# Kernel tuning notes

Measured on AMD Instinct MI355X. Metric: run time of the kernel, lower is better.

Reference implementation:

```python
import jax, jax.numpy as jnp
import numpy as np

D_MODEL = 1024
D_STATE = 16
D_CONV = 4
EXPAND = 2
D_INNER = EXPAND * D_MODEL          # 2048
DT_RANK = (D_MODEL + 15) // 16      # 64
B_SZ, L = 2, 2048


def setup_inputs() -> dict:
    key = jax.random.key(0)
    ks = jax.random.split(key, 14)
    s = 0.02
    dt_init = jax.random.uniform(ks[10], (D_INNER,), minval=1e-3, maxval=0.1)
    A = jnp.tile(jnp.arange(1, D_STATE + 1, dtype=jnp.float32)[None, :], (D_INNER, 1))
    return {
        "x_f": jax.random.normal(ks[0], (B_SZ, L, D_MODEL), jnp.float32),
        "x_h": jax.random.normal(ks[1], (B_SZ, L, D_MODEL), jnp.float32),
        "W_hf": s * jax.random.normal(ks[2], (D_MODEL, D_MODEL), jnp.float32),
        "b_hf": jnp.zeros((D_MODEL,), jnp.float32),
        "W_in": s * jax.random.normal(ks[3], (2 * D_INNER, D_MODEL), jnp.float32),
        "conv_w": s * jax.random.normal(ks[4], (D_INNER, 1, D_CONV), jnp.float32),
        "conv_b": jnp.zeros((D_INNER,), jnp.float32),
        "W_x": s * jax.random.normal(ks[5], (DT_RANK + 2 * D_STATE, D_INNER), jnp.float32),
        "W_dt": (DT_RANK ** -0.5) * jax.random.normal(ks[6], (D_INNER, DT_RANK), jnp.float32),
        "b_dt": jnp.log(jnp.expm1(dt_init)),
        "A_log": jnp.log(A),
        "D": jnp.ones((D_INNER,), jnp.float32),
        "W_out": s * jax.random.normal(ks[7], (D_MODEL, D_INNER), jnp.float32),
    }


def _mamba(x, W_in, conv_w, conv_b, W_x, W_dt, b_dt, A_log, D, W_out):
    B, Lx, _ = x.shape
    # in_proj -> x, z branches  [B, L, 2*d_inner]
    xz = jnp.einsum("bld,ed->ble", x, W_in)
    x_in, z = jnp.split(xz, 2, axis=-1)
    # causal depthwise conv1d, kernel d_conv, groups = d_inner
    x_nch = jnp.transpose(x_in, (0, 2, 1))  # [B, d_inner, L]
    x_conv = jax.lax.conv_general_dilated(
        x_nch, conv_w, window_strides=(1,), padding=[(D_CONV - 1, 0)],
        dimension_numbers=("NCH", "OIH", "NCH"), feature_group_count=D_INNER)
    x_c = jax.nn.silu(jnp.transpose(x_conv, (0, 2, 1)) + conv_b)  # [B, L, d_inner]
    # input-dependent dt, B, C
    x_dbl = jnp.einsum("ble,fe->blf", x_c, W_x)
    dt_r = x_dbl[..., :DT_RANK]
    B_ssm = x_dbl[..., DT_RANK:DT_RANK + D_STATE]          # [B, L, d_state]
    C_ssm = x_dbl[..., DT_RANK + D_STATE:]                  # [B, L, d_state]
    dt = jax.nn.softplus(jnp.einsum("blr,er->ble", dt_r, W_dt) + b_dt)  # [B, L, d_inner]
    A = -jnp.exp(A_log)  # [d_inner, d_state]

    # selective scan over time; carry h: [B, d_inner, d_state]
    def step(h, inp):
        dt_t, B_t, C_t, x_t = inp  # [B,d_inner], [B,d_state], [B,d_state], [B,d_inner]
        dA = jnp.exp(dt_t[:, :, None] * A)                       # [B, d_inner, d_state]
        dBx = dt_t[:, :, None] * B_t[:, None, :] * x_t[:, :, None]
        h = dA * h + dBx
        y_t = jnp.einsum("bes,bs->be", h, C_t)
        return h, y_t

    seq = (jnp.transpose(dt, (1, 0, 2)), jnp.transpose(B_ssm, (1, 0, 2)),
           jnp.transpose(C_ssm, (1, 0, 2)), jnp.transpose(x_c, (1, 0, 2)))
    h0 = jnp.zeros((B, D_INNER, D_STATE), x.dtype)
    _, ys = jax.lax.scan(step, h0, seq)
    y = jnp.transpose(ys, (1, 0, 2)) + D * x_c   # skip term
    y = y * jax.nn.silu(z)                        # output gate
    return jnp.einsum("ble,de->bld", y, W_out)


def reference(x_f, x_h, W_hf, b_hf, W_in, conv_w, conv_b, W_x, W_dt, b_dt, A_log, D, W_out):
    hf_gate = jax.nn.sigmoid(jnp.einsum("bld,ed->ble", x_h, W_hf) + b_hf)
    modulated = x_f * hf_gate
    return _mamba(modulated, W_in, conv_w, conv_b, W_x, W_dt, b_dt, A_log, D, W_out)
```

## Files before the change

kernel.cpp:

```cpp
#include <hip/hip_runtime.h>
#include <hip/hip_bf16.h>
#include <math.h>

#define L_SEQ  2048
#define BATCH  2
#define DMODEL 1024
#define DINNER 2048
#define DSTATE 16
#define NCHUNK 32
#define LCH    (L_SEQ / NCHUNK)

typedef __attribute__((ext_vector_type(8))) short bf16x8;
typedef __attribute__((ext_vector_type(4))) float f32x4;

__device__ __forceinline__ unsigned short f2bu(float x) {
    __hip_bfloat16 h = __float2bfloat16(x);
    return __builtin_bit_cast(unsigned short, h);
}
__device__ __forceinline__ float fast_exp2(float x) {
    float r; asm("v_exp_f32 %0, %1" : "=v"(r) : "v"(x)); return r;
}
#define LOG2E 1.44269504088896f

__global__ __launch_bounds__(256) void cvt_all(
    const float* __restrict__ Wout, const float* __restrict__ Win,
    const float* __restrict__ xh,   const float* __restrict__ Whf,
    const float* __restrict__ Wx,   const float* __restrict__ Wdt,
    __hip_bfloat16* __restrict__ dWout, __hip_bfloat16* __restrict__ dWin,
    __hip_bfloat16* __restrict__ dxh,   __hip_bfloat16* __restrict__ dWhf,
    __hip_bfloat16* __restrict__ dWx,   __hip_bfloat16* __restrict__ dWdt)
{
    int bid = blockIdx.x;
    const float* s; __hip_bfloat16* d;
    if (bid < 2048)       { s = Wout; d = dWout; }
    else if (bid < 6144)  { s = Win;  d = dWin;  bid -= 2048; }
    else if (bid < 10240) { s = xh;   d = dxh;   bid -= 6144; }
    else if (bid < 11264) { s = Whf;  d = dWhf;  bid -= 10240; }
    else if (bid < 11520) {
        bid -= 11264;
        const int i = (bid * 256 + threadIdx.x) * 4;
        const int r = i >> 11;
        ushort4 u = {0, 0, 0, 0};
        if (r < 96) {
            const float4 v = *reinterpret_cast<const float4*>(&Wx[i]);
            u.x = f2bu(v.x); u.y = f2bu(v.y); u.z = f2bu(v.z); u.w = f2bu(v.w);
        }
        *reinterpret_cast<ushort4*>(&dWx[i]) = u;
        return;
    }
    else                  { s = Wdt;  d = dWdt;  bid -= 11520; }
    const int i = (bid * 256 + threadIdx.x) * 4;
    const float4 v = *reinterpret_cast<const float4*>(&s[i]);
    ushort4 u;
    u.x = f2bu(v.x); u.y = f2bu(v.y); u.z = f2bu(v.z); u.w = f2bu(v.w);
    *reinterpret_cast<ushort4*>(&d[i]) = u;
}

template <int EPI>
__global__ __launch_bounds__(256) void mfma_gemm(
    const __hip_bfloat16* __restrict__ A, int lda,
    const __hip_bfloat16* __restrict__ Bw, int ldb,
    int ksz,
    float* __restrict__ Cf, int ldc,
    __hip_bfloat16* __restrict__ Cb,
    __hip_bfloat16* __restrict__ Cb2,
    const float* __restrict__ bias,
    const float* __restrict__ mul, int ldmul)
{
    __shared__ unsigned short As[64 * 32];
    __shared__ unsigned short Bs[128 * 32];
    const int tid = threadIdx.x;
    const int row0 = blockIdx.y * 64;
    const int col0 = blockIdx.x * 128;
    const int wid = tid >> 6, lane = tid & 63;
    const int wr = wid >> 1, wc = wid & 1;
    const int fr = lane & 15, fq = lane >> 4;
    const int kz0 = blockIdx.z * ksz;

    f32x4 acc[2][4];
#pragma unroll
    for (int i = 0; i < 2; i++)
#pragma unroll
        for (int j = 0; j < 4; j++) acc[i][j] = (f32x4){0.f, 0.f, 0.f, 0.f};

    const size_t ga  = (size_t)(row0 + (tid >> 2)) * lda + (tid & 3) * 8;
    const size_t gb0 = (size_t)(col0 + (tid >> 2)) * ldb + (tid & 3) * 8;
    const size_t gb1 = (size_t)(col0 + 64 + (tid >> 2)) * ldb + (tid & 3) * 8;
    const int nk = ksz >> 5;

    for (int kk = 0; kk < nk; kk++) {
        const int koff = kz0 + kk * 32;
#if __has_builtin(__builtin_amdgcn_global_load_lds)
        __syncthreads();
        __builtin_amdgcn_global_load_lds(
            (const __attribute__((address_space(1))) unsigned int*)(A + ga + koff),
            (__attribute__((address_space(3))) unsigned int*)&As[tid * 8], 16, 0, 0);
        __builtin_amdgcn_global_load_lds(
            (const __attribute__((address_space(1))) unsigned int*)(Bw + gb0 + koff),
            (__attribute__((address_space(3))) unsigned int*)&Bs[tid * 8], 16, 0, 0);
        __builtin_amdgcn_global_load_lds(
            (const __attribute__((address_space(1))) unsigned int*)(Bw + gb1 + koff),
            (__attribute__((address_space(3))) unsigned int*)&Bs[2048 + tid * 8], 16, 0, 0);
        __syncthreads();
#else
        const uint4 va  = *reinterpret_cast<const uint4*>(A + ga + koff);
        const uint4 vb0 = *reinterpret_cast<const uint4*>(Bw + gb0 + koff);
        const uint4 vb1 = *reinterpret_cast<const uint4*>(Bw + gb1 + koff);
        __syncthreads();
        *reinterpret_cast<uint4*>(&As[tid * 8]) = va;
        *reinterpret_cast<uint4*>(&Bs[tid * 8]) = vb0;
        *reinterpret_cast<uint4*>(&Bs[2048 + tid * 8]) = vb1;
        __syncthreads();
#endif
        bf16x8 af[2], bq[4];
#pragma unroll
        for (int rb = 0; rb < 2; rb++)
            af[rb] = *reinterpret_cast<const bf16x8*>(
                &As[(wr * 32 + rb * 16 + fr) * 32 + fq * 8]);
#pragma unroll
        for (int cb = 0; cb < 4; cb++)
            bq[cb] = *reinterpret_cast<const bf16x8*>(
                &Bs[(wc * 64 + cb * 16 + fr) * 32 + fq * 8]);
#pragma unroll
        for (int rb = 0; rb < 2; rb++)
#pragma unroll
            for (int cb = 0; cb < 4; cb++)
                acc[rb][cb] = __builtin_amdgcn_mfma_f32_16x16x32_bf16(
                    af[rb], bq[cb], acc[rb][cb], 0, 0, 0);
    }

    float* Cz = Cf;
    if (EPI == 0)
        Cz = Cf + (size_t)blockIdx.z * (size_t)(gridDim.y * 64) * ldc;
    const int r0 = row0 + wr * 32, c0 = col0 + wc * 64;
#pragma unroll
    for (int rb = 0; rb < 2; rb++)
#pragma unroll
        for (int cb = 0; cb < 4; cb++) {
            const int col = c0 + cb * 16 + fr;
#pragma unroll
            for (int j = 0; j < 4; j++) {
                const int row = r0 + rb * 16 + fq * 4 + j;
                float v = acc[rb][cb][j];
                if (EPI == 0) {
                    Cz[(size_t)row * ldc + col] = v;
                } else if (EPI == 1) {
                    v = 1.f / (1.f + __expf(-(v + bias[col])));
                    v *= mul[(size_t)row * ldmul + col];
                    Cb[(size_t)row * ldc + col] = __float2bfloat16(v);
                } else if (EPI == 2) {
                    if (col0 < 2048) Cb[(size_t)row * 2048 + col] = __float2bfloat16(v);
                    else             Cb2[(size_t)row * 2048 + col - 2048] = __float2bfloat16(v);
                } else {
                    v += bias[col];
                    v = (v > 20.f) ? v : log1pf(__expf(v));
                    Cb[(size_t)row * ldc + col] = __float2bfloat16(v);
                }
            }
        }
}

__global__ __launch_bounds__(256) void reduce_xdbl(
    const float* __restrict__ part, float* __restrict__ xdbl,
    __hip_bfloat16* __restrict__ dtr)
{
    const int i = blockIdx.x * 256 + threadIdx.x;
    float s = 0.f;
#pragma unroll
    for (int j = 0; j < 8; j++) s += part[(size_t)j * 524288 + i];
    xdbl[i] = s;
    const int col = i & 127;
    if (col < 64) dtr[((i >> 7) << 6) + col] = __float2bfloat16(s);
}

__global__ __launch_bounds__(256) void conv_silu_kernel(
    const __hip_bfloat16* __restrict__ xin_b, const float* __restrict__ cw,
    const float* __restrict__ cb, __hip_bfloat16* __restrict__ xcb)
{
    int gid = blockIdx.x * 256 + threadIdx.x;
    int e = gid & (DINNER - 1);
    int row = gid >> 11;
    int t = row & (L_SEQ - 1);
    float s = cb[e];
#pragma unroll
    for (int j = 0; j < 4; j++) {
        int tt = t - 3 + j;
        if (tt >= 0)
            s = fmaf(cw[e * 4 + j],
                     __bfloat162float(xin_b[(size_t)(row - 3 + j) * 2048 + e]), s);
    }
    xcb[(size_t)row * 2048 + e] = __float2bfloat16(s / (1.f + __expf(-s)));
}

__global__ __launch_bounds__(256) void scan_pass_a(
    const __hip_bfloat16* __restrict__ dtb, const __hip_bfloat16* __restrict__ xcb,
    const float* __restrict__ xdbl, const float* __restrict__ A_log,
    float* __restrict__ hloc, float* __restrict__ Pp)
{
    __shared__ float sB[LCH][16];
    const int tid = threadIdx.x;
    const int e = (blockIdx.x << 8) + tid;
    const int chunk = blockIdx.y;
    const int b = blockIdx.z;
    const int t0 = chunk * LCH;

    {
        const int r = tid >> 2, sl = tid & 3;
        *(float4*)&sB[r][sl * 4] =
            *(const float4*)&xdbl[(size_t)(b * L_SEQ + t0 + r) * 128 + 64 + sl * 4];
    }
    float av[16];
#pragma unroll
    for (int sq = 0; sq < 4; sq++) {
        const float4 al = *(const float4*)&A_log[e * 16 + sq * 4];
#pragma unroll
        for (int j = 0; j < 4; j++)
            av[sq * 4 + j] = -fast_exp2(((const float*)&al)[j] * LOG2E);
    }
    float h[16];
#pragma unroll
    for (int s = 0; s < 16; s++) h[s] = 0.f;
    float sdt = 0.f;
    __syncthreads();

    const size_t rb = (size_t)(b * L_SEQ + t0) * 2048 + e;
    float dtv_n = __bfloat162float(dtb[rb]);
    float xv_n = __bfloat162float(xcb[rb]);
    for (int t = 0; t < LCH; t++) {
        const float dtv = dtv_n, xv = xv_n;
        if (t + 1 < LCH) {
            dtv_n = __bfloat162float(dtb[rb + (size_t)(t + 1) * 2048]);
            xv_n = __bfloat162float(xcb[rb + (size_t)(t + 1) * 2048]);
        }
        sdt += dtv;
        const float dtx = dtv * xv;
        const float dl2 = dtv * LOG2E;
#pragma unroll
        for (int sq = 0; sq < 4; sq++) {
            const float4 B4 = *(const float4*)&sB[t][sq * 4];
#pragma unroll
            for (int j = 0; j < 4; j++) {
                const int s = sq * 4 + j;
                const float Bv = ((const float*)&B4)[j];
                h[s] = fmaf(fast_exp2(dl2 * av[s]), h[s], Bv * dtx);
            }
        }
    }
    const size_t o = (((size_t)chunk * BATCH + b) * 2048 + e) * 16;
#pragma unroll
    for (int sq = 0; sq < 4; sq++) {
        *(float4*)&hloc[o + sq * 4] =
            make_float4(h[sq * 4], h[sq * 4 + 1], h[sq * 4 + 2], h[sq * 4 + 3]);
        *(float4*)&Pp[o + sq * 4] = make_float4(
            fast_exp2(av[sq * 4] * sdt * LOG2E),
            fast_exp2(av[sq * 4 + 1] * sdt * LOG2E),
            fast_exp2(av[sq * 4 + 2] * sdt * LOG2E),
            fast_exp2(av[sq * 4 + 3] * sdt * LOG2E));
    }
}

__global__ __launch_bounds__(256) void scan_pass_b(
    const float* __restrict__ hloc, const float* __restrict__ Pp,
    float* __restrict__ h0)
{
    const int idx = blockIdx.x * 256 + threadIdx.x;
    float h = 0.f;
    h0[idx] = 0.f;
    for (int c = 0; c < NCHUNK - 1; c++) {
        h = fmaf(Pp[(size_t)c * 65536 + idx], h, hloc[(size_t)c * 65536 + idx]);
        h0[(size_t)(c + 1) * 65536 + idx] = h;
    }
}

__global__ __launch_bounds__(256) void scan_pass_c(
    const __hip_bfloat16* __restrict__ dtb, const __hip_bfloat16* __restrict__ xcb,
    const float* __restrict__ xdbl, const __hip_bfloat16* __restrict__ zb,
    const float* __restrict__ A_log, const float* __restrict__ Dw,
    const float* __restrict__ h0, __hip_bfloat16* __restrict__ yb)
{
    __shared__ float sB[LCH][16];
    __shared__ float sC[LCH][16];
    const int tid = threadIdx.x;
    const int e = (blockIdx.x << 8) + tid;
    const int chunk = blockIdx.y;
    const int b = blockIdx.z;
    const int t0 = chunk * LCH;

    {
        const int r = tid >> 2, sl = tid & 3;
        const size_t base = (size_t)(b * L_SEQ + t0 + r) * 128;
        *(float4*)&sB[r][sl * 4] = *(const float4*)&xdbl[base + 64 + sl * 4];
        *(float4*)&sC[r][sl * 4] = *(const float4*)&xdbl[base + 80 + sl * 4];
    }
    float av[16];
#pragma unroll
    for (int sq = 0; sq < 4; sq++) {
        const float4 al = *(const float4*)&A_log[e * 16 + sq * 4];
#pragma unroll
        for (int j = 0; j < 4; j++)
            av[sq * 4 + j] = -fast_exp2(((const float*)&al)[j] * LOG2E);
    }
    const float De = Dw[e];
    float h[16];
    const size_t o = (((size_t)chunk * BATCH + b) * 2048 + e) * 16;
#pragma unroll
    for (int sq = 0; sq < 4; sq++) {
        const float4 hv = *(const float4*)&h0[o + sq * 4];
        h[sq * 4] = hv.x; h[sq * 4 + 1] = hv.y;
        h[sq * 4 + 2] = hv.z; h[sq * 4 + 3] = hv.w;
    }
    __syncthreads();

    const size_t rb = (size_t)(b * L_SEQ + t0) * 2048 + e;
    float dtv_n = __bfloat162float(dtb[rb]);
    float xv_n = __bfloat162float(xcb[rb]);
    float zv_n = __bfloat162float(zb[rb]);
    for (int t = 0; t < LCH; t++) {
        const float dtv = dtv_n, xv = xv_n, zv = zv_n;
        if (t + 1 < LCH) {
            dtv_n = __bfloat162float(dtb[rb + (size_t)(t + 1) * 2048]);
            xv_n = __bfloat162float(xcb[rb + (size_t)(t + 1) * 2048]);
            zv_n = __bfloat162float(zb[rb + (size_t)(t + 1) * 2048]);
        }
        const float dtx = dtv * xv;
        const float dl2 = dtv * LOG2E;
        float yp0 = 0.f, yp1 = 0.f, yp2 = 0.f, yp3 = 0.f;
#pragma unroll
        for (int sq = 0; sq < 4; sq++) {
            const float4 B4 = *(const float4*)&sB[t][sq * 4];
            const float4 C4 = *(const float4*)&sC[t][sq * 4];
#pragma unroll
            for (int j = 0; j < 4; j++) {
                const int s = sq * 4 + j;
                const float Bv = ((const float*)&B4)[j];
                const float Cv = ((const float*)&C4)[j];
                h[s] = fmaf(fast_exp2(dl2 * av[s]), h[s], Bv * dtx);
                if (sq == 0) yp0 = fmaf(h[s], Cv, yp0);
                else if (sq == 1) yp1 = fmaf(h[s], Cv, yp1);
                else if (sq == 2) yp2 = fmaf(h[s], Cv, yp2);
                else yp3 = fmaf(h[s], Cv, yp3);
            }
        }
        float yv = (yp0 + yp1) + (yp2 + yp3);
        yv = fmaf(De, xv, yv);
        const float sig = 1.f / (1.f + __expf(-zv));
        yb[rb + (size_t)t * 2048] = __float2bfloat16(yv * zv * sig);
    }
}

extern "C" void kernel_launch(void* const* d_in, const int* in_sizes, int n_in,
                              void* d_out, int out_size, void* d_ws, size_t ws_size,
                              hipStream_t stream)
{
    const float* x_f    = (const float*)d_in[0];
    const float* x_h    = (const float*)d_in[1];
    const float* W_hf   = (const float*)d_in[2];
    const float* b_hf   = (const float*)d_in[3];
    const float* W_in   = (const float*)d_in[4];
    const float* conv_w = (const float*)d_in[5];
    const float* conv_b = (const float*)d_in[6];
    const float* W_x    = (const float*)d_in[7];
    const float* W_dt   = (const float*)d_in[8];
    const float* b_dt   = (const float*)d_in[9];
    const float* A_log  = (const float*)d_in[10];
    const float* Dw     = (const float*)d_in[11];
    const float* W_out  = (const float*)d_in[12];
    float* out = (float*)d_out;
    float* ws  = (float*)d_ws;

    __hip_bfloat16* wout_b = (__hip_bfloat16*)(ws);
    __hip_bfloat16* win_b  = (__hip_bfloat16*)(ws + 1048576);
    __hip_bfloat16* xh_b   = (__hip_bfloat16*)(ws + 3145728);
    __hip_bfloat16* whf_b  = (__hip_bfloat16*)(ws + 5242880);
    __hip_bfloat16* m_b    = (__hip_bfloat16*)(ws + 5767168);
    float*          hloc   = ws + 1048576;
    float*          Pp     = ws + 3145728;
    float*          h0     = ws + 5242880;
    __hip_bfloat16* wx_b   = (__hip_bfloat16*)(ws + 7864320);
    __hip_bfloat16* wdt_b  = (__hip_bfloat16*)(ws + 7995392);
    __hip_bfloat16* dtr_b  = (__hip_bfloat16*)(ws + 8060928);
    float*          xdbl   = ws + 10289152;
    __hip_bfloat16* xin_b  = (__hip_bfloat16*)(ws + 10813440);
    __hip_bfloat16* z_b    = (__hip_bfloat16*)(ws + 15007744);
    __hip_bfloat16* xc_b   = (__hip_bfloat16*)(ws + 19202048);
    float*          part   = ws + 23396352;
    __hip_bfloat16* dt_b   = (__hip_bfloat16*)(ws + 27590656);
    __hip_bfloat16* yb     = (__hip_bfloat16*)(ws + 31784960);

    cvt_all<<<11648, 256, 0, stream>>>(
        W_out, W_in, x_h, W_hf, W_x, W_dt,
        wout_b, win_b, xh_b, whf_b, wx_b, wdt_b);

    mfma_gemm<1><<<dim3(8, 64, 1), 256, 0, stream>>>(
        xh_b, DMODEL, whf_b, DMODEL, DMODEL,
        nullptr, DMODEL, m_b, nullptr, b_hf, x_f, DMODEL);

    mfma_gemm<2><<<dim3(32, 64, 1), 256, 0, stream>>>(
        m_b, DMODEL, win_b, DMODEL, DMODEL,
        nullptr, 2048, xin_b, z_b, nullptr, nullptr, 0);

    conv_silu_kernel<<<32768, 256, 0, stream>>>(
        xin_b, conv_w, conv_b, xc_b);

    mfma_gemm<0><<<dim3(1, 64, 8), 256, 0, stream>>>(
        xc_b, DINNER, wx_b, DINNER, 256,
        part, 128, nullptr, nullptr, nullptr, nullptr, 0);
    reduce_xdbl<<<2048, 256, 0, stream>>>(part, xdbl, dtr_b);

    mfma_gemm<3><<<dim3(16, 64, 1), 256, 0, stream>>>(
        dtr_b, 64, wdt_b, 64, 64,
        nullptr, 2048, dt_b, nullptr, b_dt, nullptr, 0);

    scan_pass_a<<<dim3(8, NCHUNK - 1, BATCH), 256, 0, stream>>>(
        dt_b, xc_b, xdbl, A_log, hloc, Pp);
    scan_pass_b<<<256, 256, 0, stream>>>(hloc, Pp, h0);
    scan_pass_c<<<dim3(8, NCHUNK, BATCH), 256, 0, stream>>>(
        dt_b, xc_b, xdbl, z_b, A_log, Dw, h0, yb);

    mfma_gemm<0><<<dim3(8, 64, 1), 256, 0, stream>>>(
        yb, DINNER, wout_b, DINNER, DINNER,
        out, DMODEL, nullptr, nullptr, nullptr, nullptr, 0);
}
```

Baseline: 304.2 us.

## Enlarge GEMM row tiles, vectorize conv, double scan chunks, store scan state in bf16

The MFMA GEMM block tile grows from 64x128 to 128x128, with each wave computing a 64x64 sub-tile, to raise operand reuse and halve the grid. The depthwise conv kernel now handles two channels per thread with paired bf16 loads and stores. The chunked scan uses 64 chunks instead of 32 to expose more parallelism in passes A and C. The per-chunk states, decay products and carried-in states are now stored as bf16 to cut their traffic. Trade-offs: more accumulator registers per GEMM thread, fewer GEMM blocks to fill the GPU, and bf16 rounding of the recurrent state, which can hurt accuracy.

```diff
diff --git a/kernel.cpp b/kernel.cpp
--- a/kernel.cpp
+++ b/kernel.cpp
@@ -7,7 +7,7 @@
 #define DMODEL 1024
 #define DINNER 2048
 #define DSTATE 16
-#define NCHUNK 32
+#define NCHUNK 64
 #define LCH    (L_SEQ / NCHUNK)
 
 typedef __attribute__((ext_vector_type(8))) short bf16x8;
@@ -16,6 +16,10 @@
 __device__ __forceinline__ unsigned short f2bu(float x) {
     __hip_bfloat16 h = __float2bfloat16(x);
     return __builtin_bit_cast(unsigned short, h);
+}
+__device__ __forceinline__ float bu2f(unsigned short u) {
+    __hip_bfloat16 h = __builtin_bit_cast(__hip_bfloat16, u);
+    return __bfloat162float(h);
 }
 __device__ __forceinline__ float fast_exp2(float x) {
     float r; asm("v_exp_f32 %0, %1" : "=v"(r) : "v"(x)); return r;
@@ -67,25 +71,27 @@
     const float* __restrict__ bias,
     const float* __restrict__ mul, int ldmul)
 {
-    __shared__ unsigned short As[64 * 32];
+    __shared__ unsigned short As[128 * 32];
     __shared__ unsigned short Bs[128 * 32];
     const int tid = threadIdx.x;
-    const int row0 = blockIdx.y * 64;
+    const int row0 = blockIdx.y * 128;
     const int col0 = blockIdx.x * 128;
     const int wid = tid >> 6, lane = tid & 63;
     const int wr = wid >> 1, wc = wid & 1;
     const int fr = lane & 15, fq = lane >> 4;
     const int kz0 = blockIdx.z * ksz;
 
-    f32x4 acc[2][4];
-#pragma unroll
-    for (int i = 0; i < 2; i++)
+    f32x4 acc[4][4];
+#pragma unroll
+    for (int i = 0; i < 4; i++)
 #pragma unroll
         for (int j = 0; j < 4; j++) acc[i][j] = (f32x4){0.f, 0.f, 0.f, 0.f};
 
-    const size_t ga  = (size_t)(row0 + (tid >> 2)) * lda + (tid & 3) * 8;
-    const size_t gb0 = (size_t)(col0 + (tid >> 2)) * ldb + (tid & 3) * 8;
-    const size_t gb1 = (size_t)(col0 + 64 + (tid >> 2)) * ldb + (tid & 3) * 8;
+    const int i0 = tid, i1 = tid + 256;
+    const size_t ga0 = (size_t)(row0 + (i0 >> 2)) * lda + (i0 & 3) * 8;
+    const size_t ga1 = (size_t)(row0 + (i1 >> 2)) * lda + (i1 & 3) * 8;
+    const size_t gb0 = (size_t)(col0 + (i0 >> 2)) * ldb + (i0 & 3) * 8;
+    const size_t gb1 = (size_t)(col0 + (i1 >> 2)) * ldb + (i1 & 3) * 8;
     const int nk = ksz >> 5;
 
     for (int kk = 0; kk < nk; kk++) {
@@ -93,36 +99,41 @@
 #if __has_builtin(__builtin_amdgcn_global_load_lds)
         __syncthreads();
         __builtin_amdgcn_global_load_lds(
-            (const __attribute__((address_space(1))) unsigned int*)(A + ga + koff),
-            (__attribute__((address_space(3))) unsigned int*)&As[tid * 8], 16, 0, 0);
+            (const __attribute__((address_space(1))) unsigned int*)(A + ga0 + koff),
+            (__attribute__((address_space(3))) unsigned int*)&As[i0 * 8], 16, 0, 0);
+        __builtin_amdgcn_global_load_lds(
+            (const __attribute__((address_space(1))) unsigned int*)(A + ga1 + koff),
+            (__attribute__((address_space(3))) unsigned int*)&As[i1 * 8], 16, 0, 0);
         __builtin_amdgcn_global_load_lds(
             (const __attribute__((address_space(1))) unsigned int*)(Bw + gb0 + koff),
-            (__attribute__((address_space(3))) unsigned int*)&Bs[tid * 8], 16, 0, 0);
+            (__attribute__((address_space(3))) unsigned int*)&Bs[i0 * 8], 16, 0, 0);
         __builtin_amdgcn_global_load_lds(
             (const __attribute__((address_space(1))) unsigned int*)(Bw + gb1 + koff),
-            (__attribute__((address_space(3))) unsigned int*)&Bs[2048 + tid * 8], 16, 0, 0);
+            (__attribute__((address_space(3))) unsigned int*)&Bs[i1 * 8], 16, 0, 0);
         __syncthreads();
 #else
-        const uint4 va  = *reinterpret_cast<const uint4*>(A + ga + koff);
+        const uint4 va0 = *reinterpret_cast<const uint4*>(A + ga0 + koff);
+        const uint4 va1 = *reinterpret_cast<const uint4*>(A + ga1 + koff);
         const uint4 vb0 = *reinterpret_cast<const uint4*>(Bw + gb0 + koff);
         const uint4 vb1 = *reinterpret_cast<const uint4*>(Bw + gb1 + koff);
         __syncthreads();
-        *reinterpret_cast<uint4*>(&As[tid * 8]) = va;
-        *reinterpret_cast<uint4*>(&Bs[tid * 8]) = vb0;
-        *reinterpret_cast<uint4*>(&Bs[2048 + tid * 8]) = vb1;
+        *reinterpret_cast<uint4*>(&As[i0 * 8]) = va0;
+        *reinterpret_cast<uint4*>(&As[i1 * 8]) = va1;
+        *reinterpret_cast<uint4*>(&Bs[i0 * 8]) = vb0;
+        *reinterpret_cast<uint4*>(&Bs[i1 * 8]) = vb1;
         __syncthreads();
 #endif
-        bf16x8 af[2], bq[4];
-#pragma unroll
-        for (int rb = 0; rb < 2; rb++)
+        bf16x8 af[4], bq[4];
+#pragma unroll
+        for (int rb = 0; rb < 4; rb++)
             af[rb] = *reinterpret_cast<const bf16x8*>(
-                &As[(wr * 32 + rb * 16 + fr) * 32 + fq * 8]);
+                &As[(wr * 64 + rb * 16 + fr) * 32 + fq * 8]);
 #pragma unroll
         for (int cb = 0; cb < 4; cb++)
             bq[cb] = *reinterpret_cast<const bf16x8*>(
                 &Bs[(wc * 64 + cb * 16 + fr) * 32 + fq * 8]);
 #pragma unroll
-        for (int rb = 0; rb < 2; rb++)
+        for (int rb = 0; rb < 4; rb++)
 #pragma unroll
             for (int cb = 0; cb < 4; cb++)
                 acc[rb][cb] = __builtin_amdgcn_mfma_f32_16x16x32_bf16(
@@ -131,10 +142,10 @@
 
     float* Cz = Cf;
     if (EPI == 0)
-        Cz = Cf + (size_t)blockIdx.z * (size_t)(gridDim.y * 64) * ldc;
-    const int r0 = row0 + wr * 32, c0 = col0 + wc * 64;
-#pragma unroll
-    for (int rb = 0; rb < 2; rb++)
+        Cz = Cf + (size_t)blockIdx.z * (size_t)(gridDim.y * 128) * ldc;
+    const int r0 = row0 + wr * 64, c0 = col0 + wc * 64;
+#pragma unroll
+    for (int rb = 0; rb < 4; rb++)
 #pragma unroll
         for (int cb = 0; cb < 4; cb++) {
             const int col = c0 + cb * 16 + fr;
@@ -177,25 +188,33 @@
     const __hip_bfloat16* __restrict__ xin_b, const float* __restrict__ cw,
     const float* __restrict__ cb, __hip_bfloat16* __restrict__ xcb)
 {
-    int gid = blockIdx.x * 256 + threadIdx.x;
-    int e = gid & (DINNER - 1);
-    int row = gid >> 11;
-    int t = row & (L_SEQ - 1);
-    float s = cb[e];
+    const int gid = blockIdx.x * 256 + threadIdx.x;
+    const int ep = gid & 1023;
+    const int row = gid >> 10;
+    const int t = row & (L_SEQ - 1);
+    const int e = ep * 2;
+    const float2 b2 = *reinterpret_cast<const float2*>(&cb[e]);
+    float s0 = b2.x, s1 = b2.y;
 #pragma unroll
     for (int j = 0; j < 4; j++) {
-        int tt = t - 3 + j;
-        if (tt >= 0)
-            s = fmaf(cw[e * 4 + j],
-                     __bfloat162float(xin_b[(size_t)(row - 3 + j) * 2048 + e]), s);
-    }
-    xcb[(size_t)row * 2048 + e] = __float2bfloat16(s / (1.f + __expf(-s)));
+        const int tt = t - 3 + j;
+        if (tt >= 0) {
+            const __hip_bfloat162 v = *reinterpret_cast<const __hip_bfloat162*>(
+                &xin_b[(size_t)(row - 3 + j) * 2048 + e]);
+            s0 = fmaf(cw[e * 4 + j],     __bfloat162float(v.x), s0);
+            s1 = fmaf(cw[e * 4 + 4 + j], __bfloat162float(v.y), s1);
+        }
+    }
+    __hip_bfloat162 o;
+    o.x = __float2bfloat16(s0 / (1.f + __expf(-s0)));
+    o.y = __float2bfloat16(s1 / (1.f + __expf(-s1)));
+    *reinterpret_cast<__hip_bfloat162*>(&xcb[(size_t)row * 2048 + e]) = o;
 }
 
 __global__ __launch_bounds__(256) void scan_pass_a(
     const __hip_bfloat16* __restrict__ dtb, const __hip_bfloat16* __restrict__ xcb,
     const float* __restrict__ xdbl, const float* __restrict__ A_log,
-    float* __restrict__ hloc, float* __restrict__ Pp)
+    __hip_bfloat16* __restrict__ hloc, __hip_bfloat16* __restrict__ Pp)
 {
     __shared__ float sB[LCH][16];
     const int tid = threadIdx.x;
@@ -204,7 +223,7 @@
     const int b = blockIdx.z;
     const int t0 = chunk * LCH;
 
-    {
+    if (tid < LCH * 4) {
         const int r = tid >> 2, sl = tid & 3;
         *(float4*)&sB[r][sl * 4] =
             *(const float4*)&xdbl[(size_t)(b * L_SEQ + t0 + r) * 128 + 64 + sl * 4];
@@ -249,26 +268,30 @@
     const size_t o = (((size_t)chunk * BATCH + b) * 2048 + e) * 16;
 #pragma unroll
     for (int sq = 0; sq < 4; sq++) {
-        *(float4*)&hloc[o + sq * 4] =
-            make_float4(h[sq * 4], h[sq * 4 + 1], h[sq * 4 + 2], h[sq * 4 + 3]);
-        *(float4*)&Pp[o + sq * 4] = make_float4(
-            fast_exp2(av[sq * 4] * sdt * LOG2E),
-            fast_exp2(av[sq * 4 + 1] * sdt * LOG2E),
-            fast_exp2(av[sq * 4 + 2] * sdt * LOG2E),
-            fast_exp2(av[sq * 4 + 3] * sdt * LOG2E));
+        ushort4 uh, up;
+        uh.x = f2bu(h[sq * 4]);     uh.y = f2bu(h[sq * 4 + 1]);
+        uh.z = f2bu(h[sq * 4 + 2]); uh.w = f2bu(h[sq * 4 + 3]);
+        up.x = f2bu(fast_exp2(av[sq * 4] * sdt * LOG2E));
+        up.y = f2bu(fast_exp2(av[sq * 4 + 1] * sdt * LOG2E));
+        up.z = f2bu(fast_exp2(av[sq * 4 + 2] * sdt * LOG2E));
+        up.w = f2bu(fast_exp2(av[sq * 4 + 3] * sdt * LOG2E));
+        *(ushort4*)&hloc[o + sq * 4] = uh;
+        *(ushort4*)&Pp[o + sq * 4] = up;
     }
 }
 
 __global__ __launch_bounds__(256) void scan_pass_b(
-    const float* __restrict__ hloc, const float* __restrict__ Pp,
-    float* __restrict__ h0)
+    const __hip_bfloat16* __restrict__ hloc, const __hip_bfloat16* __restrict__ Pp,
+    __hip_bfloat16* __restrict__ h0)
 {
     const int idx = blockIdx.x * 256 + threadIdx.x;
     float h = 0.f;
-    h0[idx] = 0.f;
+    h0[idx] = __float2bfloat16(0.f);
     for (int c = 0; c < NCHUNK - 1; c++) {
-        h = fmaf(Pp[(size_t)c * 65536 + idx], h, hloc[(size_t)c * 65536 + idx]);
-        h0[(size_t)(c + 1) * 65536 + idx] = h;
+        const float P = __bfloat162float(Pp[(size_t)c * 65536 + idx]);
+        const float hl = __bfloat162float(hloc[(size_t)c * 65536 + idx]);
+        h = fmaf(P, h, hl);
+        h0[(size_t)(c + 1) * 65536 + idx] = __float2bfloat16(h);
     }
 }
 
@@ -276,7 +299,7 @@
     const __hip_bfloat16* __restrict__ dtb, const __hip_bfloat16* __restrict__ xcb,
     const float* __restrict__ xdbl, const __hip_bfloat16* __restrict__ zb,
     const float* __restrict__ A_log, const float* __restrict__ Dw,
-    const float* __restrict__ h0, __hip_bfloat16* __restrict__ yb)
+    const __hip_bfloat16* __restrict__ h0, __hip_bfloat16* __restrict__ yb)
 {
     __shared__ float sB[LCH][16];
     __shared__ float sC[LCH][16];
@@ -286,11 +309,15 @@
     const int b = blockIdx.z;
     const int t0 = chunk * LCH;
 
-    {
+    if (tid < LCH * 4) {
         const int r = tid >> 2, sl = tid & 3;
-        const size_t base = (size_t)(b * L_SEQ + t0 + r) * 128;
-        *(float4*)&sB[r][sl * 4] = *(const float4*)&xdbl[base + 64 + sl * 4];
-        *(float4*)&sC[r][sl * 4] = *(const float4*)&xdbl[base + 80 + sl * 4];
+        *(float4*)&sB[r][sl * 4] =
+            *(const float4*)&xdbl[(size_t)(b * L_SEQ + t0 + r) * 128 + 64 + sl * 4];
+    } else if (tid < LCH * 8) {
+        const int t2 = tid - LCH * 4;
+        const int r = t2 >> 2, sl = t2 & 3;
+        *(float4*)&sC[r][sl * 4] =
+            *(const float4*)&xdbl[(size_t)(b * L_SEQ + t0 + r) * 128 + 80 + sl * 4];
     }
     float av[16];
 #pragma unroll
@@ -305,9 +332,9 @@
     const size_t o = (((size_t)chunk * BATCH + b) * 2048 + e) * 16;
 #pragma unroll
     for (int sq = 0; sq < 4; sq++) {
-        const float4 hv = *(const float4*)&h0[o + sq * 4];
-        h[sq * 4] = hv.x; h[sq * 4 + 1] = hv.y;
-        h[sq * 4 + 2] = hv.z; h[sq * 4 + 3] = hv.w;
+        const ushort4 hv = *(const ushort4*)&h0[o + sq * 4];
+        h[sq * 4]     = bu2f(hv.x); h[sq * 4 + 1] = bu2f(hv.y);
+        h[sq * 4 + 2] = bu2f(hv.z); h[sq * 4 + 3] = bu2f(hv.w);
     }
     __syncthreads();
 
@@ -373,9 +400,9 @@
     __hip_bfloat16* xh_b   = (__hip_bfloat16*)(ws + 3145728);
     __hip_bfloat16* whf_b  = (__hip_bfloat16*)(ws + 5242880);
     __hip_bfloat16* m_b    = (__hip_bfloat16*)(ws + 5767168);
-    float*          hloc   = ws + 1048576;
-    float*          Pp     = ws + 3145728;
-    float*          h0     = ws + 5242880;
+    __hip_bfloat16* hloc   = (__hip_bfloat16*)(ws + 1048576);
+    __hip_bfloat16* Pp     = (__hip_bfloat16*)(ws + 3145728);
+    __hip_bfloat16* h0     = (__hip_bfloat16*)(ws + 5242880);
     __hip_bfloat16* wx_b   = (__hip_bfloat16*)(ws + 7864320);
     __hip_bfloat16* wdt_b  = (__hip_bfloat16*)(ws + 7995392);
     __hip_bfloat16* dtr_b  = (__hip_bfloat16*)(ws + 8060928);
@@ -391,23 +418,23 @@
         W_out, W_in, x_h, W_hf, W_x, W_dt,
         wout_b, win_b, xh_b, whf_b, wx_b, wdt_b);
 
-    mfma_gemm<1><<<dim3(8, 64, 1), 256, 0, stream>>>(
+    mfma_gemm<1><<<dim3(8, 32, 1), 256, 0, stream>>>(
         xh_b, DMODEL, whf_b, DMODEL, DMODEL,
         nullptr, DMODEL, m_b, nullptr, b_hf, x_f, DMODEL);
 
-    mfma_gemm<2><<<dim3(32, 64, 1), 256, 0, stream>>>(
+    mfma_gemm<2><<<dim3(32, 32, 1), 256, 0, stream>>>(
         m_b, DMODEL, win_b, DMODEL, DMODEL,
         nullptr, 2048, xin_b, z_b, nullptr, nullptr, 0);
 
-    conv_silu_kernel<<<32768, 256, 0, stream>>>(
+    conv_silu_kernel<<<16384, 256, 0, stream>>>(
         xin_b, conv_w, conv_b, xc_b);
 
-    mfma_gemm<0><<<dim3(1, 64, 8), 256, 0, stream>>>(
+    mfma_gemm<0><<<dim3(1, 32, 8), 256, 0, stream>>>(
         xc_b, DINNER, wx_b, DINNER, 256,
         part, 128, nullptr, nullptr, nullptr, nullptr, 0);
     reduce_xdbl<<<2048, 256, 0, stream>>>(part, xdbl, dtr_b);
 
-    mfma_gemm<3><<<dim3(16, 64, 1), 256, 0, stream>>>(
+    mfma_gemm<3><<<dim3(16, 32, 1), 256, 0, stream>>>(
         dtr_b, 64, wdt_b, 64, 64,
         nullptr, 2048, dt_b, nullptr, b_dt, nullptr, 0);
 
@@ -417,7 +444,7 @@
     scan_pass_c<<<dim3(8, NCHUNK, BATCH), 256, 0, stream>>>(
         dt_b, xc_b, xdbl, z_b, A_log, Dw, h0, yb);
 
-    mfma_gemm<0><<<dim3(8, 64, 1), 256, 0, stream>>>(
+    mfma_gemm<0><<<dim3(8, 32, 1), 256, 0, stream>>>(
         yb, DINNER, wout_b, DINNER, DINNER,
         out, DMODEL, nullptr, nullptr, nullptr, nullptr, 0);
 }
```

Measured after the change: 328.8 us. +8.1%, slower.
